# Kernel tuning notes

Measured on AMD Instinct MI355X. Metric: run time of the kernel, lower is better.

Reference implementation:

```python
import jax, jax.numpy as jnp
import numpy as np

N_NODES = 100000
N_EDGES = 3200000
HIDDEN = 128


def _linear_params(key, din, dout):
    s = 1.0 / np.sqrt(din)
    kw, kb = jax.random.split(key)
    W = jax.random.uniform(kw, (dout, din), minval=-s, maxval=s, dtype=jnp.float32)
    b = jax.random.uniform(kb, (dout,), minval=-s, maxval=s, dtype=jnp.float32)
    return W, b


def setup_inputs() -> dict:
    key = jax.random.key(0)
    ks = jax.random.split(key, 9)
    x = jax.random.normal(ks[0], (N_NODES, 5), dtype=jnp.float32)
    edge_index = jax.random.randint(ks[1], (2, N_EDGES), 0, N_NODES, dtype=jnp.int64)
    W1, b1 = _linear_params(ks[2], 5, 64)
    W2, b2 = _linear_params(ks[3], 64, HIDDEN)
    W3, b3 = _linear_params(ks[4], HIDDEN, HIDDEN)
    W4, b4 = _linear_params(ks[5], HIDDEN, HIDDEN)
    Wc1, bc1 = _linear_params(ks[6], HIDDEN, HIDDEN)
    Wc2, bc2 = _linear_params(ks[7], HIDDEN, HIDDEN)
    W5, b5 = _linear_params(ks[8], HIDDEN, 60)
    return {"x": x, "edge_index": edge_index,
            "W1": W1, "b1": b1, "W2": W2, "b2": b2,
            "W3": W3, "b3": b3, "W4": W4, "b4": b4,
            "Wc1": Wc1, "bc1": bc1, "Wc2": Wc2, "bc2": bc2,
            "W5": W5, "b5": b5}


def gcn_conv(x, edge_index, W, b):
    """GCNConv: self-loops + symmetric deg^-1/2 normalization."""
    n = x.shape[0]
    loop = jnp.arange(n, dtype=edge_index.dtype)
    src = jnp.concatenate([edge_index[0], loop])  # [E+N]
    dst = jnp.concatenate([edge_index[1], loop])  # [E+N]
    h = x @ W.T                                    # [N, H]
    ones = jnp.ones_like(dst, dtype=h.dtype)
    deg = jax.ops.segment_sum(ones, dst, num_segments=n)         # [N]
    dinv = jnp.where(deg > 0, jax.lax.rsqrt(deg), 0.0)
    norm = dinv[src] * dinv[dst]                                  # [E+N]
    msg = h[src] * norm[:, None]                                  # gather + scale
    out = jax.ops.segment_sum(msg, dst, num_segments=n)           # scatter-add
    return out + b


def reference(x, edge_index, W1, b1, W2, b2, W3, b3, W4, b4,
              Wc1, bc1, Wc2, bc2, W5, b5):
    h = jax.nn.relu(x @ W1.T + b1)
    h = jax.nn.relu(h @ W2.T + b2)
    h = jax.nn.relu(h @ W3.T + b3) + h
    h = jax.nn.relu(h @ W4.T + b4) + h
    h = jax.nn.relu(gcn_conv(h, edge_index, Wc1, bc1))
    h = jax.nn.relu(gcn_conv(h, edge_index, Wc2, bc2))
    return h @ W5.T + b5  # [N, 60]
```

## Files before the change

### kernel.cpp

```cpp
#include <hip/hip_runtime.h>
#include <hip/hip_fp16.h>

typedef __attribute__((ext_vector_type(8))) short bf16x8;
typedef __attribute__((ext_vector_type(4))) float f32x4;

__device__ __forceinline__ float frelu(float v){ return fmaxf(v, 0.f); }
__device__ __forceinline__ short f2bf(float f){
  unsigned u = __float_as_uint(f);
  unsigned r = (u + 0x7fffu + ((u>>16)&1u)) >> 16;
  return (short)r;
}
__device__ __forceinline__ float bf2f(short h){
  return __uint_as_float(((unsigned)(unsigned short)h) << 16);
}

__global__ __launch_bounds__(256) void k_lin5(const float* __restrict__ x,
    const float* __restrict__ W1, const float* __restrict__ b1,
    float* __restrict__ out, int n)
{
  int t = blockIdx.x*256 + threadIdx.x;
  int node = t >> 6, c = t & 63;
  if (node >= n) return;
  float acc = b1[c];
  const float* xr = x + (size_t)node*5;
  const float* wr = W1 + c*5;
  #pragma unroll
  for (int k=0;k<5;k++) acc = fmaf(xr[k], wr[k], acc);
  out[(size_t)node*64 + c] = frelu(acc);
}

template<int K, int BN, int COLS_REAL, int PRE, int EPI, int WRG, int WCG>
__global__ __launch_bounds__(512) void k_mgemm(const float* __restrict__ A,
    const float* __restrict__ W, const float* __restrict__ bpre,
    const float* __restrict__ bpost, const float* __restrict__ dscale,
    float* __restrict__ Out, int n)
{
  constexpr int BM = WRG*64;
  __shared__ __align__(16) short sAh[BM*32];
  __shared__ __align__(16) short sAl[BM*32];
  __shared__ __align__(16) short sWh[BN*32];
  __shared__ __align__(16) short sWl[BN*32];

  const int tid = threadIdx.x;
  const int nb0 = blockIdx.x * BM;
  const int l = tid & 63;
  const int w = tid >> 6;
  const int wr = w % WRG;
  const int wc = w / WRG;
  const int lrow = l & 15;
  const int koct = l >> 4;

  f32x4 acc[4][4];
  #pragma unroll
  for (int i=0;i<4;i++)
    #pragma unroll
    for (int j=0;j<4;j++) acc[i][j] = (f32x4){0.f,0.f,0.f,0.f};

  for (int kc = 0; kc < K/32; ++kc) {
    if (kc) __syncthreads();
    #pragma unroll
    for (int t = 0; t < BM/128; ++t) {
      int idx = tid + t*512;
      int row = idx >> 2, kq = idx & 3;
      int node = nb0 + row;
      float a[8];
      if (node < n) {
        const float* g = A + (size_t)node*K + kc*32 + kq*8;
        float4 v0 = *(const float4*)g;
        float4 v1 = *(const float4*)(g+4);
        a[0]=v0.x; a[1]=v0.y; a[2]=v0.z; a[3]=v0.w;
        a[4]=v1.x; a[5]=v1.y; a[6]=v1.z; a[7]=v1.w;
      } else {
        #pragma unroll
        for (int j=0;j<8;j++) a[j]=0.f;
      }
      if constexpr (PRE == 1) {
        const float* bp = bpre + kc*32 + kq*8;
        float4 b0 = *(const float4*)bp;
        float4 b1 = *(const float4*)(bp+4);
        a[0]=frelu(a[0]+b0.x); a[1]=frelu(a[1]+b0.y);
        a[2]=frelu(a[2]+b0.z); a[3]=frelu(a[3]+b0.w);
        a[4]=frelu(a[4]+b1.x); a[5]=frelu(a[5]+b1.y);
        a[6]=frelu(a[6]+b1.z); a[7]=frelu(a[7]+b1.w);
      }
      union { short s[8]; bf16x8 v; } ph, pl;
      #pragma unroll
      for (int j=0;j<8;j++) {
        short h = f2bf(a[j]);
        ph.s[j] = h;
        pl.s[j] = f2bf(a[j] - bf2f(h));
      }
      int byte = (row<<6) | (kq<<4);
      byte ^= (row&7)<<4;
      *(bf16x8*)((char*)sAh + byte) = ph.v;
      *(bf16x8*)((char*)sAl + byte) = pl.v;
    }
    if (BN*4 >= 512 || tid < BN*4) {
      int idx = tid;
      int c = idx >> 2, kq = idx & 3;
      float a[8];
      if (COLS_REAL == BN || c < COLS_REAL) {
        const float* g = W + (size_t)c*K + kc*32 + kq*8;
        float4 v0 = *(const float4*)g;
        float4 v1 = *(const float4*)(g+4);
        a[0]=v0.x; a[1]=v0.y; a[2]=v0.z; a[3]=v0.w;
        a[4]=v1.x; a[5]=v1.y; a[6]=v1.z; a[7]=v1.w;
      } else {
        #pragma unroll
        for (int j=0;j<8;j++) a[j]=0.f;
      }
      union { short s[8]; bf16x8 v; } ph, pl;
      #pragma unroll
      for (int j=0;j<8;j++) {
        short h = f2bf(a[j]);
        ph.s[j] = h;
        pl.s[j] = f2bf(a[j] - bf2f(h));
      }
      int byte = (c<<6) | (kq<<4);
      byte ^= (c&7)<<4;
      *(bf16x8*)((char*)sWh + byte) = ph.v;
      *(bf16x8*)((char*)sWl + byte) = pl.v;
    }
    __syncthreads();
    bf16x8 fah[4], fal[4], fwh[4], fwl[4];
    #pragma unroll
    for (int rf=0; rf<4; ++rf) {
      int row = wr*64 + rf*16 + lrow;
      int byte = (row<<6) | (koct<<4);
      byte ^= (row&7)<<4;
      fah[rf] = *(const bf16x8*)((const char*)sAh + byte);
      fal[rf] = *(const bf16x8*)((const char*)sAl + byte);
    }
    #pragma unroll
    for (int cf=0; cf<4; ++cf) {
      int c = wc*64 + cf*16 + lrow;
      int byte = (c<<6) | (koct<<4);
      byte ^= (c&7)<<4;
      fwh[cf] = *(const bf16x8*)((const char*)sWh + byte);
      fwl[cf] = *(const bf16x8*)((const char*)sWl + byte);
    }
    #pragma unroll
    for (int rf=0; rf<4; ++rf)
      #pragma unroll
      for (int cf=0; cf<4; ++cf) {
        acc[rf][cf] = __builtin_amdgcn_mfma_f32_16x16x32_bf16(fah[rf], fwh[cf], acc[rf][cf], 0,0,0);
        acc[rf][cf] = __builtin_amdgcn_mfma_f32_16x16x32_bf16(fah[rf], fwl[cf], acc[rf][cf], 0,0,0);
        acc[rf][cf] = __builtin_amdgcn_mfma_f32_16x16x32_bf16(fal[rf], fwh[cf], acc[rf][cf], 0,0,0);
      }
  }
  const int crow = (l >> 4) * 4;
  float bpc[4];
  if constexpr (EPI==1 || EPI==2 || EPI==3) {
    #pragma unroll
    for (int cf=0; cf<4; ++cf) {
      int col = wc*64 + cf*16 + (l & 15);
      bpc[cf] = (COLS_REAL == BN || col < COLS_REAL) ? bpost[col] : 0.f;
    }
  }
  #pragma unroll
  for (int rf=0; rf<4; ++rf) {
    #pragma unroll
    for (int reg=0; reg<4; ++reg) {
      int row = wr*64 + rf*16 + crow + reg;
      int node = nb0 + row;
      if (node >= n) continue;
      float ds = 1.f;
      if constexpr (EPI==4 || EPI==5) ds = dscale[node];
      #pragma unroll
      for (int cf=0; cf<4; ++cf) {
        int col = wc*64 + cf*16 + (l & 15);
        if (COLS_REAL != BN && col >= COLS_REAL) continue;
        float v = acc[rf][cf][reg];
        if constexpr (EPI==1) v += bpc[cf];
        if constexpr (EPI==2) v = frelu(v + bpc[cf]);
        if constexpr (EPI==3) v = frelu(v + bpc[cf]) + A[(size_t)node*K + col];
        if constexpr (EPI==4) v *= ds;
        if constexpr (EPI==5) {
          v *= ds;
          ((__half*)Out)[(size_t)node*COLS_REAL + col] = __float2half_rn(v);
        } else {
          Out[(size_t)node*COLS_REAL + col] = v;
        }
      }
    }
  }
}

__global__ __launch_bounds__(512) void k_zero512(int* __restrict__ a, int m){
  int i = threadIdx.x; if (i<m) a[i]=0;
}
__global__ __launch_bounds__(512) void k_bhist(const int* __restrict__ dst,
    int* __restrict__ bcnt, int E, int nbuck){
  __shared__ int l[512];
  int tid = threadIdx.x;
  if (tid < nbuck) l[tid]=0;
  __syncthreads();
  for (int e = blockIdx.x*512 + tid; e < E; e += gridDim.x*512)
    atomicAdd(&l[((unsigned)dst[e])>>8], 1);
  __syncthreads();
  if (tid < nbuck && l[tid]) atomicAdd(&bcnt[tid], l[tid]);
}
__global__ __launch_bounds__(512) void k_bscan(const int* __restrict__ bcnt,
    int* __restrict__ bbase, int* __restrict__ bcur, int nbuck){
  __shared__ int sc[512];
  int tid = threadIdx.x;
  int v = (tid<nbuck) ? bcnt[tid] : 0;
  sc[tid]=v; __syncthreads();
  for (int off=1; off<512; off<<=1){
    int t = (tid>=off)? sc[tid-off] : 0;
    __syncthreads();
    sc[tid]+=t;
    __syncthreads();
  }
  if (tid<nbuck){ bbase[tid]=sc[tid]-v; bcur[tid]=sc[tid]-v; }
  if (tid==nbuck-1) bbase[nbuck]=sc[tid];
}
__global__ __launch_bounds__(512) void k_bscatter(const int* __restrict__ src,
    const int* __restrict__ dst, int* __restrict__ bcur,
    unsigned* __restrict__ sorted, int E, int nbuck)
{
  __shared__ int lcnt[512];
  __shared__ int lbase[512];
  int tid = threadIdx.x;
  if (tid < nbuck) lcnt[tid]=0;
  __syncthreads();
  int e0 = blockIdx.x*8192;
  int e1 = min(e0+8192, E);
  for (int e = e0+tid; e < e1; e += 512)
    atomicAdd(&lcnt[((unsigned)dst[e])>>8], 1);
  __syncthreads();
  if (tid < nbuck) lbase[tid] = lcnt[tid] ? atomicAdd(&bcur[tid], lcnt[tid]) : 0;
  __syncthreads();
  if (tid < nbuck) lcnt[tid]=0;
  __syncthreads();
  for (int e = e0+tid; e < e1; e += 512){
    int d = dst[e];
    int k = ((unsigned)d)>>8;
    int pos = lbase[k] + atomicAdd(&lcnt[k], 1);
    sorted[pos] = (((unsigned)src[e])<<8) | ((unsigned)d & 255u);
  }
}
__global__ __launch_bounds__(512) void k_finesort(unsigned* __restrict__ sorted,
    const int* __restrict__ bbase, int* __restrict__ cend,
    float* __restrict__ dinv, int n, int* __restrict__ fb)
{
  constexpr int CAP = 16384;
  __shared__ int lsorted[CAP];
  __shared__ int cnt[256], cur[256], sc[256];
  const int k = blockIdx.x;
  const int base = bbase[k], endb = bbase[k+1];
  const int m = endb - base;
  const int node0 = k<<8;
  const int tid = threadIdx.x;
  if (tid<256) cnt[tid]=0;
  __syncthreads();
  for (int i=tid; i<m; i+=512) atomicAdd(&cnt[sorted[base+i]&255u], 1);
  __syncthreads();
  int v=0;
  if (tid<256){ v=cnt[tid]; sc[tid]=v; }
  __syncthreads();
  for (int off=1; off<256; off<<=1){
    int t=0;
    if (tid>=off && tid<256) t=sc[tid-off];
    __syncthreads();
    if (tid<256) sc[tid]+=t;
    __syncthreads();
  }
  if (tid<256){
    cur[tid]=sc[tid]-v;
    int node = node0 + tid;
    if (node < n){
      cend[node] = base + sc[tid];
      dinv[node] = rsqrtf((float)v + 1.0f);
    }
  }
  __syncthreads();
  if (m <= CAP){
    for (int i=tid; i<m; i+=512){
      unsigned p = sorted[base+i];
      int pos = atomicAdd(&cur[p&255u], 1);
      lsorted[pos] = (int)(p>>8);
    }
    __syncthreads();
    for (int i=tid; i<m; i+=512) sorted[base+i] = (unsigned)lsorted[i];
  } else {
    for (int i=tid; i<m; i+=512) fb[base+i] = (int)sorted[base+i];
    __syncthreads();
    for (int i=tid; i<m; i+=512){
      unsigned p = (unsigned)fb[base+i];
      int pos = atomicAdd(&cur[p&255u], 1);
      sorted[base+pos] = p>>8;
    }
  }
}

__global__ __launch_bounds__(256) void k_agg(const int* __restrict__ cend,
    const unsigned* __restrict__ srcs, const float* __restrict__ dinv,
    const __half* __restrict__ tp, float* __restrict__ out, int n)
{
  int node = blockIdx.x*4 + (threadIdx.x>>6);
  if (node >= n) return;
  const int lane = threadIdx.x & 63;
  const __half2* tpp = (const __half2*)tp;
  int beg = (node==0) ? 0 : cend[node-1];
  int end = cend[node];
  float2 acc;
  { __half2 h = tpp[(size_t)node*64 + lane]; acc.x = __low2float(h); acc.y = __high2float(h); }
  int e = beg;
  for (; e+4<=end; e+=4){
    unsigned s0=srcs[e], s1=srcs[e+1], s2=srcs[e+2], s3=srcs[e+3];
    __half2 h0 = tpp[(size_t)s0*64 + lane];
    __half2 h1 = tpp[(size_t)s1*64 + lane];
    __half2 h2 = tpp[(size_t)s2*64 + lane];
    __half2 h3 = tpp[(size_t)s3*64 + lane];
    acc.x += (__low2float(h0)+__low2float(h1)) + (__low2float(h2)+__low2float(h3));
    acc.y += (__high2float(h0)+__high2float(h1)) + (__high2float(h2)+__high2float(h3));
  }
  for (; e<end; ++e){
    __half2 h = tpp[(size_t)srcs[e]*64 + lane];
    acc.x += __low2float(h); acc.y += __high2float(h);
  }
  float di = dinv[node];
  float2 r; r.x = acc.x*di; r.y = acc.y*di;
  *(float2*)(out + (size_t)node*128 + (lane<<1)) = r;
}

extern "C" void kernel_launch(void* const* d_in, const int* in_sizes, int n_in,
                              void* d_out, int out_size, void* d_ws, size_t ws_size,
                              hipStream_t stream)
{
  const float* x   = (const float*)d_in[0];
  const int*   ei  = (const int*)d_in[1];
  const float *W1=(const float*)d_in[2],  *b1=(const float*)d_in[3];
  const float *W2=(const float*)d_in[4],  *b2=(const float*)d_in[5];
  const float *W3=(const float*)d_in[6],  *b3=(const float*)d_in[7];
  const float *W4=(const float*)d_in[8],  *b4=(const float*)d_in[9];
  const float *Wc1=(const float*)d_in[10],*bc1=(const float*)d_in[11];
  const float *Wc2=(const float*)d_in[12],*bc2=(const float*)d_in[13];
  const float *W5=(const float*)d_in[14], *b5=(const float*)d_in[15];
  float* out = (float*)d_out;

  const int n = in_sizes[0] / 5;
  const int E = in_sizes[1] / 2;
  const int* esrc = ei;
  const int* edst = ei + E;
  const int nbuck = (n + 255) >> 8;

  dim3 B256(256), B512(512);
  const int G256 = (n + 255)/256;
  const int G512 = (n + 511)/512;

  char* p = (char*)d_ws;
  float* hA    = (float*)p;           p += (size_t)n*128*4;
  float* hB    = (float*)p;           p += (size_t)n*128*4;
  float* dinv  = (float*)p;           p += (size_t)n*4;
  int*   cend  = (int*)p;             p += (size_t)n*4;
  unsigned* sortedp = (unsigned*)p;   p += (size_t)E*4;
  int*   bcnt  = (int*)p;             p += 512*4;
  int*   bbase = (int*)p;             p += 513*4;
  int*   bcur  = (int*)p;             p += 512*4;

  k_lin5<<<dim3((n*64 + 255)/256), B256, 0, stream>>>(x, W1, b1, hA, n);
  k_mgemm<64,128,128,0,2,4,2><<<dim3(G256), B512, 0, stream>>>(hA, W2, nullptr, b2, nullptr, hB, n);
  k_mgemm<128,128,128,0,3,4,2><<<dim3(G256), B512, 0, stream>>>(hB, W3, nullptr, b3, nullptr, hA, n);
  k_mgemm<128,128,128,0,3,4,2><<<dim3(G256), B512, 0, stream>>>(hA, W4, nullptr, b4, nullptr, hB, n);

  k_zero512<<<dim3(1), B512, 0, stream>>>(bcnt, nbuck);
  k_bhist<<<dim3(512), B512, 0, stream>>>(edst, bcnt, E, nbuck);
  k_bscan<<<dim3(1), B512, 0, stream>>>(bcnt, bbase, bcur, nbuck);
  k_bscatter<<<dim3((E + 8191)/8192), B512, 0, stream>>>(esrc, edst, bcur, sortedp, E, nbuck);
  k_finesort<<<dim3(nbuck), B512, 0, stream>>>(sortedp, bbase, cend, dinv, n, (int*)hA);

  k_mgemm<128,128,128,0,5,4,2><<<dim3(G256), B512, 0, stream>>>(hB, Wc1, nullptr, nullptr, dinv, hA, n);
  k_agg<<<dim3((n+3)/4), B256, 0, stream>>>(cend, sortedp, dinv, (const __half*)hA, hB, n);

  k_mgemm<128,128,128,1,5,4,2><<<dim3(G256), B512, 0, stream>>>(hB, Wc2, bc1, nullptr, dinv, hA, n);
  k_agg<<<dim3((n+3)/4), B256, 0, stream>>>(cend, sortedp, dinv, (const __half*)hA, hB, n);

  k_mgemm<128,64,60,1,1,8,1><<<dim3(G512), B512, 0, stream>>>(hB, W5, bc2, b5, nullptr, out, n);
}
```

Measured before the change: 475.8 us.

## Split aggregation into feature chunks with 8-edge parallel gather per wavefront

The aggregation kernel is restructured so each wavefront handles one 16-feature chunk of a node and processes 8 edges at once (8 lanes per edge, 8 half2 channels each), then reduces across edge groups with xor shuffles. Blocks are interleaved by chunk so the 8 chunks of a node group run as separate blocks. The goal is more independent memory requests in flight per wave than the old one-row-per-wave loop. The cost is redundant reads of the srcs indices (eight times over), narrower 32-byte gather segments, masked tail iterations and shuffle reduction overhead.

```diff
diff --git a/kernel.cpp b/kernel.cpp
--- a/kernel.cpp
+++ b/kernel.cpp
@@ -294,35 +294,43 @@
   }
 }
 
-__global__ __launch_bounds__(256) void k_agg(const int* __restrict__ cend,
+__global__ __launch_bounds__(512) void k_aggc(const int* __restrict__ cend,
     const unsigned* __restrict__ srcs, const float* __restrict__ dinv,
     const __half* __restrict__ tp, float* __restrict__ out, int n)
 {
-  int node = blockIdx.x*4 + (threadIdx.x>>6);
+  const int chunk = blockIdx.x & 7;
+  const int node = (blockIdx.x >> 3)*8 + (threadIdx.x >> 6);
   if (node >= n) return;
-  const int lane = threadIdx.x & 63;
+  const int l = threadIdx.x & 63;
+  const int eg = l >> 3, ch = l & 7;
   const __half2* tpp = (const __half2*)tp;
-  int beg = (node==0) ? 0 : cend[node-1];
-  int end = cend[node];
-  float2 acc;
-  { __half2 h = tpp[(size_t)node*64 + lane]; acc.x = __low2float(h); acc.y = __high2float(h); }
-  int e = beg;
-  for (; e+4<=end; e+=4){
-    unsigned s0=srcs[e], s1=srcs[e+1], s2=srcs[e+2], s3=srcs[e+3];
-    __half2 h0 = tpp[(size_t)s0*64 + lane];
-    __half2 h1 = tpp[(size_t)s1*64 + lane];
-    __half2 h2 = tpp[(size_t)s2*64 + lane];
-    __half2 h3 = tpp[(size_t)s3*64 + lane];
-    acc.x += (__low2float(h0)+__low2float(h1)) + (__low2float(h2)+__low2float(h3));
-    acc.y += (__high2float(h0)+__high2float(h1)) + (__high2float(h2)+__high2float(h3));
-  }
-  for (; e<end; ++e){
-    __half2 h = tpp[(size_t)srcs[e]*64 + lane];
+  const int c0 = chunk*8;
+  const int beg = (node==0) ? 0 : cend[node-1];
+  const int end = cend[node];
+  const int deg = end - beg;
+  float2 acc = {0.f, 0.f};
+  const int iters = (deg + 7) >> 3;
+  for (int i=0; i<iters; ++i){
+    int e = beg + i*8 + eg;
+    int ec = min(e, end-1);
+    unsigned s = srcs[ec];
+    __half2 h = tpp[(size_t)s*64 + c0 + ch];
+    float m = (e < end) ? 1.f : 0.f;
+    acc.x = fmaf(__low2float(h), m, acc.x);
+    acc.y = fmaf(__high2float(h), m, acc.y);
+  }
+  #pragma unroll
+  for (int msk=8; msk<64; msk<<=1){
+    acc.x += __shfl_xor(acc.x, msk, 64);
+    acc.y += __shfl_xor(acc.y, msk, 64);
+  }
+  if (eg == 0){
+    __half2 h = tpp[(size_t)node*64 + c0 + ch];
     acc.x += __low2float(h); acc.y += __high2float(h);
-  }
-  float di = dinv[node];
-  float2 r; r.x = acc.x*di; r.y = acc.y*di;
-  *(float2*)(out + (size_t)node*128 + (lane<<1)) = r;
+    float di = dinv[node];
+    float2 r; r.x = acc.x*di; r.y = acc.y*di;
+    *(float2*)(out + (size_t)node*128 + (c0+ch)*2) = r;
+  }
 }
 
 extern "C" void kernel_launch(void* const* d_in, const int* in_sizes, int n_in,
@@ -349,6 +357,7 @@
   dim3 B256(256), B512(512);
   const int G256 = (n + 255)/256;
   const int G512 = (n + 511)/512;
+  const int GAGG = 8 * ((n + 7)/8);
 
   char* p = (char*)d_ws;
   float* hA    = (float*)p;           p += (size_t)n*128*4;
@@ -372,10 +381,10 @@
   k_finesort<<<dim3(nbuck), B512, 0, stream>>>(sortedp, bbase, cend, dinv, n, (int*)hA);
 
   k_mgemm<128,128,128,0,5,4,2><<<dim3(G256), B512, 0, stream>>>(hB, Wc1, nullptr, nullptr, dinv, hA, n);
-  k_agg<<<dim3((n+3)/4), B256, 0, stream>>>(cend, sortedp, dinv, (const __half*)hA, hB, n);
+  k_aggc<<<dim3(GAGG), B512, 0, stream>>>(cend, sortedp, dinv, (const __half*)hA, hB, n);
 
   k_mgemm<128,128,128,1,5,4,2><<<dim3(G256), B512, 0, stream>>>(hB, Wc2, bc1, nullptr, dinv, hA, n);
-  k_agg<<<dim3((n+3)/4), B256, 0, stream>>>(cend, sortedp, dinv, (const __half*)hA, hB, n);
+  k_aggc<<<dim3(GAGG), B512, 0, stream>>>(cend, sortedp, dinv, (const __half*)hA, hB, n);
 
   k_mgemm<128,64,60,1,1,8,1><<<dim3(G512), B512, 0, stream>>>(hB, W5, bc2, b5, nullptr, out, n);
 }
```

Result: slower. 1.165 ms (+144.8%).

## Fuse input MLP and first GCN transform into one LDS-resident megakernel

Applied to the files above, without the earlier changes.

Replaces the separate lin5 kernel and four GEMM launches (W2, W3, W4, Wc1) with a single kernel that keeps each 32-node tile's activations in shared memory as split bf16 hi/lo pairs across all layers. The Wc1 output is scaled by dinv and written as fp16. A small pre-pass converts the weights once into a swizzled hi/lo bf16 layout, so the megakernel can stream them straight into LDS. This removes the global-memory round trips of the intermediate 128-wide activations between layers, at the cost of smaller tiles, weights reloaded per kc chunk in every block, and many syncthreads.

```diff
diff --git a/kernel.cpp b/kernel.cpp
--- a/kernel.cpp
+++ b/kernel.cpp
@@ -12,21 +12,6 @@
 }
 __device__ __forceinline__ float bf2f(short h){
   return __uint_as_float(((unsigned)(unsigned short)h) << 16);
-}
-
-__global__ __launch_bounds__(256) void k_lin5(const float* __restrict__ x,
-    const float* __restrict__ W1, const float* __restrict__ b1,
-    float* __restrict__ out, int n)
-{
-  int t = blockIdx.x*256 + threadIdx.x;
-  int node = t >> 6, c = t & 63;
-  if (node >= n) return;
-  float acc = b1[c];
-  const float* xr = x + (size_t)node*5;
-  const float* wr = W1 + c*5;
-  #pragma unroll
-  for (int k=0;k<5;k++) acc = fmaf(xr[k], wr[k], acc);
-  out[(size_t)node*64 + c] = frelu(acc);
 }
 
 template<int K, int BN, int COLS_REAL, int PRE, int EPI, int WRG, int WCG>
@@ -186,6 +171,162 @@
   }
 }
 
+__global__ __launch_bounds__(256) void k_wsplit(const float* __restrict__ W2,
+    const float* __restrict__ W3, const float* __restrict__ W4,
+    const float* __restrict__ Wc1, short* __restrict__ whi, short* __restrict__ wlo)
+{
+  int idx = blockIdx.x*256 + threadIdx.x;
+  if (idx >= 57344) return;
+  const float* src; int e, c, k, cbase;
+  if (idx < 8192){ src=W2; e=idx; c=e>>6; k=e&63; cbase=0; }
+  else if (idx < 24576){ src=W3; e=idx-8192; c=e>>7; k=e&127; cbase=8192; }
+  else if (idx < 40960){ src=W4; e=idx-24576; c=e>>7; k=e&127; cbase=24576; }
+  else { src=Wc1; e=idx-40960; c=e>>7; k=e&127; cbase=40960; }
+  float v = src[e];
+  short h = f2bf(v);
+  short lo = f2bf(v - bf2f(h));
+  int byte = ((c<<6) | ((k&31)<<1)) ^ ((c&7)<<4);
+  int pos = cbase + (k>>5)*4096 + (byte>>1);
+  whi[pos] = h; wlo[pos] = lo;
+}
+
+__global__ __launch_bounds__(256) void k_mega(const float* __restrict__ x,
+    const float* __restrict__ W1, const float* __restrict__ b1,
+    const float* __restrict__ b2, const float* __restrict__ b3,
+    const float* __restrict__ b4, const short* __restrict__ whi,
+    const short* __restrict__ wlo, const float* __restrict__ dinv,
+    __half* __restrict__ tp1, int n)
+{
+  __shared__ __align__(16) short sWh[4096], sWl[4096];
+  __shared__ __align__(16) short bAh[4096], bAl[4096];
+  __shared__ __align__(16) short bBh[4096], bBl[4096];
+  __shared__ float sx[160];
+  __shared__ float sW1[320];
+  __shared__ float sb1[64];
+  const int tid = threadIdx.x;
+  const int nb0 = blockIdx.x*32;
+
+  if (tid < 160){ int row = tid/5, col = tid - row*5; int node = nb0 + row;
+    sx[tid] = (node < n) ? x[(size_t)node*5 + col] : 0.f; }
+  if (tid < 64) sb1[tid] = b1[tid];
+  for (int i = tid; i < 320; i += 256) sW1[i] = W1[i];
+  __syncthreads();
+
+  {
+    int row = tid >> 3, c0 = (tid & 7)*8;
+    float xr[5];
+    #pragma unroll
+    for (int k=0;k<5;k++) xr[k] = sx[row*5+k];
+    #pragma unroll
+    for (int j=0;j<8;j++){
+      int c = c0 + j;
+      float a = sb1[c];
+      #pragma unroll
+      for (int k=0;k<5;k++) a = fmaf(xr[k], sW1[c*5+k], a);
+      a = frelu(a);
+      short h = f2bf(a), lo = f2bf(a - bf2f(h));
+      int byte = ((c>>5)<<11) + ((((row<<6)|((c&31)<<1))) ^ ((row&7)<<4));
+      *(short*)((char*)bAh + byte) = h;
+      *(short*)((char*)bAl + byte) = lo;
+    }
+  }
+
+  const int l = tid & 63, w = tid >> 6;
+  const int wr = w >> 1, wc = w & 1;
+  const int lrow = l & 15, koct = l >> 4;
+  const int arow = wr*16 + lrow;
+  const int abyteNoKc = ((arow<<6)|(koct<<4)) ^ ((arow&7)<<4);
+  int wbyte[4];
+  #pragma unroll
+  for (int cf=0; cf<4; ++cf){
+    int c = wc*64 + cf*16 + lrow;
+    wbyte[cf] = ((c<<6)|(koct<<4)) ^ ((c&7)<<4);
+  }
+  f32x4 acc[4];
+  float res[4][4];
+
+  auto run_layer = [&](const short* inH, const short* inL, int woff, int nkc){
+    #pragma unroll
+    for (int cf=0; cf<4; ++cf) acc[cf] = (f32x4){0.f,0.f,0.f,0.f};
+    for (int kc=0; kc<nkc; ++kc){
+      __syncthreads();
+      {
+        const bf16x8* gh = (const bf16x8*)(whi + woff + kc*4096);
+        const bf16x8* gl = (const bf16x8*)(wlo + woff + kc*4096);
+        ((bf16x8*)sWh)[tid*2]   = gh[tid*2];
+        ((bf16x8*)sWh)[tid*2+1] = gh[tid*2+1];
+        ((bf16x8*)sWl)[tid*2]   = gl[tid*2];
+        ((bf16x8*)sWl)[tid*2+1] = gl[tid*2+1];
+      }
+      __syncthreads();
+      int ab = (kc<<11) + abyteNoKc;
+      bf16x8 fah = *(const bf16x8*)((const char*)inH + ab);
+      bf16x8 fal = *(const bf16x8*)((const char*)inL + ab);
+      #pragma unroll
+      for (int cf=0; cf<4; ++cf){
+        bf16x8 fwh = *(const bf16x8*)((const char*)sWh + wbyte[cf]);
+        bf16x8 fwl = *(const bf16x8*)((const char*)sWl + wbyte[cf]);
+        acc[cf] = __builtin_amdgcn_mfma_f32_16x16x32_bf16(fah, fwh, acc[cf], 0,0,0);
+        acc[cf] = __builtin_amdgcn_mfma_f32_16x16x32_bf16(fah, fwl, acc[cf], 0,0,0);
+        acc[cf] = __builtin_amdgcn_mfma_f32_16x16x32_bf16(fal, fwh, acc[cf], 0,0,0);
+      }
+    }
+  };
+  auto store_buf = [&](short* outH, short* outL, int cf, int reg, float v){
+    int row = wr*16 + koct*4 + reg;
+    int col = wc*64 + cf*16 + lrow;
+    short h = f2bf(v), lo = f2bf(v - bf2f(h));
+    int byte = ((col>>5)<<11) + (((row<<6)|((col&31)<<1)) ^ ((row&7)<<4));
+    *(short*)((char*)outH + byte) = h;
+    *(short*)((char*)outL + byte) = lo;
+  };
+
+  run_layer(bAh, bAl, 0, 2);
+  #pragma unroll
+  for (int cf=0; cf<4; ++cf){
+    float bb = b2[wc*64 + cf*16 + lrow];
+    #pragma unroll
+    for (int reg=0; reg<4; ++reg){
+      float v = frelu(acc[cf][reg] + bb);
+      res[cf][reg] = v;
+      store_buf(bBh, bBl, cf, reg, v);
+    }
+  }
+  run_layer(bBh, bBl, 8192, 4);
+  #pragma unroll
+  for (int cf=0; cf<4; ++cf){
+    float bb = b3[wc*64 + cf*16 + lrow];
+    #pragma unroll
+    for (int reg=0; reg<4; ++reg){
+      float v = frelu(acc[cf][reg] + bb) + res[cf][reg];
+      res[cf][reg] = v;
+      store_buf(bAh, bAl, cf, reg, v);
+    }
+  }
+  run_layer(bAh, bAl, 24576, 4);
+  #pragma unroll
+  for (int cf=0; cf<4; ++cf){
+    float bb = b4[wc*64 + cf*16 + lrow];
+    #pragma unroll
+    for (int reg=0; reg<4; ++reg){
+      float v = frelu(acc[cf][reg] + bb) + res[cf][reg];
+      store_buf(bBh, bBl, cf, reg, v);
+    }
+  }
+  run_layer(bBh, bBl, 40960, 4);
+  #pragma unroll
+  for (int reg=0; reg<4; ++reg){
+    int row = wr*16 + koct*4 + reg;
+    int node = nb0 + row;
+    float di = dinv[min(node, n-1)];
+    #pragma unroll
+    for (int cf=0; cf<4; ++cf){
+      int col = wc*64 + cf*16 + lrow;
+      if (node < n) tp1[(size_t)node*128 + col] = __float2half_rn(acc[cf][reg]*di);
+    }
+  }
+}
+
 __global__ __launch_bounds__(512) void k_zero512(int* __restrict__ a, int m){
   int i = threadIdx.x; if (i<m) a[i]=0;
 }
@@ -359,11 +500,8 @@
   int*   bcnt  = (int*)p;             p += 512*4;
   int*   bbase = (int*)p;             p += 513*4;
   int*   bcur  = (int*)p;             p += 512*4;
-
-  k_lin5<<<dim3((n*64 + 255)/256), B256, 0, stream>>>(x, W1, b1, hA, n);
-  k_mgemm<64,128,128,0,2,4,2><<<dim3(G256), B512, 0, stream>>>(hA, W2, nullptr, b2, nullptr, hB, n);
-  k_mgemm<128,128,128,0,3,4,2><<<dim3(G256), B512, 0, stream>>>(hB, W3, nullptr, b3, nullptr, hA, n);
-  k_mgemm<128,128,128,0,3,4,2><<<dim3(G256), B512, 0, stream>>>(hA, W4, nullptr, b4, nullptr, hB, n);
+  short* whi   = (short*)p;           p += 57344*2;
+  short* wlo   = (short*)p;           p += 57344*2;
 
   k_zero512<<<dim3(1), B512, 0, stream>>>(bcnt, nbuck);
   k_bhist<<<dim3(512), B512, 0, stream>>>(edst, bcnt, E, nbuck);
@@ -371,7 +509,10 @@
   k_bscatter<<<dim3((E + 8191)/8192), B512, 0, stream>>>(esrc, edst, bcur, sortedp, E, nbuck);
   k_finesort<<<dim3(nbuck), B512, 0, stream>>>(sortedp, bbase, cend, dinv, n, (int*)hA);
 
-  k_mgemm<128,128,128,0,5,4,2><<<dim3(G256), B512, 0, stream>>>(hB, Wc1, nullptr, nullptr, dinv, hA, n);
+  k_wsplit<<<dim3(224), B256, 0, stream>>>(W2, W3, W4, Wc1, whi, wlo);
+
+  k_mega<<<dim3((n + 31)/32), B256, 0, stream>>>(x, W1, b1, b2, b3, b4,
+                                                 whi, wlo, dinv, (__half*)hA, n);
   k_agg<<<dim3((n+3)/4), B256, 0, stream>>>(cend, sortedp, dinv, (const __half*)hA, hB, n);
 
   k_mgemm<128,128,128,1,5,4,2><<<dim3(G256), B512, 0, stream>>>(hB, Wc2, bc1, nullptr, dinv, hA, n);
```

New measurement: 448.8 us. 1.06x faster.
